# Optimization experiments

Hardware: AMD Instinct MI355X
Metric: run time of the kernel (lower is better)

Reference implementation:

```python
import jax, jax.numpy as jnp
import numpy as np

B, NL, EL, D, H = 16, 512, 1024, 256, 8
HD = D // H
EPS = 1e-5


def _layernorm(x, g, b):
    mu = jnp.mean(x, axis=-1, keepdims=True)
    var = jnp.mean(jnp.square(x - mu), axis=-1, keepdims=True)
    return (x - mu) * jax.lax.rsqrt(var + EPS) * g + b


def setup_inputs() -> dict:
    key = jax.random.key(0)
    ks = jax.random.split(key, 12)
    # xavier-uniform-ish scale for projections
    def xavier(k, shape):
        fan_in, fan_out = shape[0], shape[1]
        lim = float(np.sqrt(6.0 / (fan_in + fan_out)))
        return jax.random.uniform(k, shape, jnp.float32, -lim, lim)
    return {
        "node_x": jax.random.normal(ks[0], (B, NL, D), jnp.float32),
        "edge_x": jax.random.normal(ks[1], (B, EL, D), jnp.float32),
        "node_mask": jnp.zeros((B, NL, NL + EL), dtype=bool),
        "W1": xavier(ks[2], (D, 3 * D)),
        "b1": jnp.zeros((3 * D,), jnp.float32),
        "W2": xavier(ks[3], (D, 2 * D)),
        "b2": jnp.zeros((2 * D,), jnp.float32),
        "lin1_w": xavier(ks[4], (D, D)),
        "lin1_b": jnp.zeros((D,), jnp.float32),
        "lin2_w": xavier(ks[5], (D, D)),
        "lin2_b": jnp.zeros((D,), jnp.float32),
        "ln1_g": jnp.ones((D,), jnp.float32),
        "ln1_b": jnp.zeros((D,), jnp.float32),
        "ln2_g": jnp.ones((D,), jnp.float32),
        "ln2_b": jnp.zeros((D,), jnp.float32),
    }


def reference(node_x, edge_x, node_mask, W1, b1, W2, b2,
              lin1_w, lin1_b, lin2_w, lin2_b, ln1_g, ln1_b, ln2_g, ln2_b):
    b, nl, d = node_x.shape
    el = edge_x.shape[1]
    scaling = float(HD) ** -0.5
    # projections (batch-first; equivalent to the seq-first torch code)
    qkv = node_x @ W1 + b1                       # [b, nl, 3d]
    q, k_node, v_node = jnp.split(qkv, 3, axis=-1)
    kv_e = edge_x @ W2 + b2                      # [b, el, 2d]
    k_edge, v_edge = jnp.split(kv_e, 2, axis=-1)
    k = jnp.concatenate([k_node, k_edge], axis=1)  # [b, nl+el, d]
    v = jnp.concatenate([v_node, v_edge], axis=1)
    # split heads
    qh = q.reshape(b, nl, H, HD)
    kh = k.reshape(b, nl + el, H, HD)
    vh = v.reshape(b, nl + el, H, HD)
    scores = jnp.einsum('bqhd,bkhd->bhqk', qh, kh) * scaling  # [b,h,nl,nl+el]
    scores = jnp.where(node_mask[:, None, :, :], -jnp.inf, scores)
    attn = jax.nn.softmax(scores, axis=-1)
    ctx = jnp.einsum('bhqk,bkhd->bqhd', attn, vh).reshape(b, nl, d)
    # residual + LN1 (dropout is identity in eval/p=0)
    x = _layernorm(node_x + ctx, ln1_g, ln1_b)
    # FFN (relu) + residual + LN2; torch Linear: y = x @ W.T + b
    ff = jax.nn.relu(x @ lin1_w.T + lin1_b) @ lin2_w.T + lin2_b
    x = _layernorm(x + ff, ln2_g, ln2_b)
    return x
```

## Files before the change

### kernel.cpp

```cpp
#include <hip/hip_runtime.h>
#include <hip/hip_bf16.h>

using u16 = unsigned short;
using u32 = unsigned int;
using u64 = unsigned long long;
typedef __attribute__((ext_vector_type(8))) short short8;
typedef __attribute__((ext_vector_type(4))) float f32x4;
typedef __attribute__((ext_vector_type(16))) float f32x16;
typedef __attribute__((ext_vector_type(4))) u32 u32x4;

constexpr int kB = 16, kNL = 512, kEL = 1024, kD = 256, kH = 8, kHD = 32;
constexpr int kS = kNL + kEL;
constexpr int kM1 = kB * kNL;
constexpr float kScale = 0.17677669529663687f;
constexpr float kLog2e = 1.4426950408889634f;
constexpr float kQS = kScale * kLog2e;
constexpr float kEps = 1e-5f;

__device__ __forceinline__ u16 f2bh(float f) {
    __hip_bfloat16 h = __float2bfloat16(f);
    return __builtin_bit_cast(u16, h);
}
__device__ __forceinline__ u32 packbf(float lo, float hi) {
    return (__float_as_uint(hi) & 0xffff0000u) | (__float_as_uint(lo) >> 16);
}
__device__ __forceinline__ void load4(const float* p, float* o) {
    float4 v = *reinterpret_cast<const float4*>(p);
    o[0] = v.x; o[1] = v.y; o[2] = v.z; o[3] = v.w;
}
__device__ __forceinline__ f32x16 fzero16() {
    f32x16 z;
    #pragma unroll
    for (int i = 0; i < 16; ++i) z[i] = 0.f;
    return z;
}

__global__ __launch_bounds__(256) void prep_k(
    const float* __restrict__ W1, const float* __restrict__ W2,
    const float* __restrict__ l1w, const float* __restrict__ l2w,
    const float* __restrict__ nodef, const float* __restrict__ edgef,
    const u32* __restrict__ mask,
    u16* __restrict__ Wt1, u16* __restrict__ Wt2,
    u16* __restrict__ Wt3, u16* __restrict__ Wt4,
    u16* __restrict__ nodeb, u16* __restrict__ edgeb,
    u32* __restrict__ Mw)
{
    const int vb = blockIdx.x, t = threadIdx.x;
    if (vb < 320) {
        const int sec = (vb < 192) ? 0 : 1;
        const int bid = (sec == 0) ? vb : vb - 192;
        const int N = (sec == 0) ? 768 : 512;
        const float* src = (sec == 0) ? W1 : W2;
        u16* dst = (sec == 0) ? Wt1 : Wt2;
        const int tk = bid / (N / 32), tn = bid % (N / 32);
        __shared__ float T[32][33];
        {
            const int k = t >> 3, n4 = (t & 7) * 4;
            float v[4]; load4(src + (size_t)(tk * 32 + k) * N + tn * 32 + n4, v);
            T[n4+0][k] = v[0]; T[n4+1][k] = v[1]; T[n4+2][k] = v[2]; T[n4+3][k] = v[3];
        }
        __syncthreads();
        {
            const int n = t >> 3, k4 = (t & 7) * 4;
            ushort4 o = {f2bh(T[n][k4+0]), f2bh(T[n][k4+1]),
                         f2bh(T[n][k4+2]), f2bh(T[n][k4+3])};
            *reinterpret_cast<ushort4*>(dst + (size_t)(tn*32 + n) * 256 + tk*32 + k4) = o;
        }
        return;
    }
    if (vb < 448) {
        const int sec = (vb < 384) ? 0 : 1;
        const int bid = (sec == 0) ? vb - 320 : vb - 384;
        const float* src = (sec == 0) ? l1w : l2w;
        u16* dst = (sec == 0) ? Wt3 : Wt4;
        const int i = bid * 1024 + t * 4;
        float v[4]; load4(src + i, v);
        ushort4 o = {f2bh(v[0]), f2bh(v[1]), f2bh(v[2]), f2bh(v[3])};
        *reinterpret_cast<ushort4*>(dst + i) = o;
        return;
    }
    if (vb < 6592) {
        const int sec = (vb < 2496) ? 0 : 1;
        const int bid = (sec == 0) ? vb - 448 : vb - 2496;
        const float* src = (sec == 0) ? nodef : edgef;
        u16* dst = (sec == 0) ? nodeb : edgeb;
        const int i = bid * 1024 + t * 4;
        float v[4]; load4(src + i, v);
        ushort4 o = {f2bh(v[0]), f2bh(v[1]), f2bh(v[2]), f2bh(v[3])};
        *reinterpret_cast<ushort4*>(dst + i) = o;
        return;
    }
    {
        const int bid = vb - 6592;
        const int row = bid * 4 + (t >> 6);
        const int l = t & 63;
        const u32* mr = mask + (size_t)row * (kS / 4);
        u32 word = 0;
        #pragma unroll
        for (int k = 0; k < 6; ++k) {
            const u32 v = mr[k * 64 + l];
            const u64 bal = __ballot(v != 0);
            word |= (((bal) & 0xffffull) ? 1u : 0u) << (k * 4 + 0);
            word |= (((bal >> 16) & 0xffffull) ? 1u : 0u) << (k * 4 + 1);
            word |= (((bal >> 32) & 0xffffull) ? 1u : 0u) << (k * 4 + 2);
            word |= (((bal >> 48) & 0xffffull) ? 1u : 0u) << (k * 4 + 3);
        }
        if (l == 0) Mw[row] = word;
    }
}

template<int N, int K, int MODE>
__device__ __forceinline__ void gemm_body128(
    const u16* __restrict__ A, const u16* __restrict__ Wt,
    const float* __restrict__ bias,
    void* __restrict__ o0v, void* __restrict__ o1v, void* __restrict__ o2v,
    int bx, int by, u16* AsB, u16* BsB)
{
    const int t = threadIdx.x;
    const int w = t >> 6, l = t & 63;
    const int wr = w >> 1, wc = w & 1;
    const int lq = l & 15, lg = l >> 4;
    const int bm = bx * 128, bn = by * 128;

    f32x4 acc[4][4];
    #pragma unroll
    for (int mi = 0; mi < 4; ++mi)
        #pragma unroll
        for (int ni = 0; ni < 4; ++ni) acc[mi][ni] = (f32x4){0.f, 0.f, 0.f, 0.f};

    auto stage = [&](int buf, int kk) {
        u16* As = AsB + buf * (128 * 40);
        u16* Bs = BsB + buf * (128 * 40);
        const int m = t >> 1, kh = (t & 1) * 16;
        const u16* ap = A + (size_t)(bm + m) * K + kk + kh;
        *reinterpret_cast<short8*>(&As[m * 40 + kh]) = *reinterpret_cast<const short8*>(ap);
        *reinterpret_cast<short8*>(&As[m * 40 + kh + 8]) = *reinterpret_cast<const short8*>(ap + 8);
        const u16* bp = Wt + (size_t)(bn + m) * K + kk + kh;
        *reinterpret_cast<short8*>(&Bs[m * 40 + kh]) = *reinterpret_cast<const short8*>(bp);
        *reinterpret_cast<short8*>(&Bs[m * 40 + kh + 8]) = *reinterpret_cast<const short8*>(bp + 8);
    };

    stage(0, 0);
    __syncthreads();
    int buf = 0;
    for (int kk = 0; kk < K; kk += 32) {
        if (kk + 32 < K) stage(buf ^ 1, kk + 32);
        const u16* As = AsB + buf * (128 * 40);
        const u16* Bs = BsB + buf * (128 * 40);
        short8 bf[4];
        #pragma unroll
        for (int ni = 0; ni < 4; ++ni)
            bf[ni] = *reinterpret_cast<const short8*>(
                &Bs[(wc * 64 + ni * 16 + lq) * 40 + lg * 8]);
        #pragma unroll
        for (int mi = 0; mi < 4; ++mi) {
            const short8 af = *reinterpret_cast<const short8*>(
                &As[(wr * 64 + mi * 16 + lq) * 40 + lg * 8]);
            #pragma unroll
            for (int ni = 0; ni < 4; ++ni)
                acc[mi][ni] = __builtin_amdgcn_mfma_f32_16x16x32_bf16(
                    af, bf[ni], acc[mi][ni], 0, 0, 0);
        }
        __syncthreads();
        buf ^= 1;
    }

    #pragma unroll
    for (int mi = 0; mi < 4; ++mi) {
        #pragma unroll
        for (int ni = 0; ni < 4; ++ni) {
            const int cg = bn + wc * 64 + ni * 16 + lq;
            const int rg0 = bm + wr * 64 + mi * 16 + lg * 4;
            const float bv = bias[cg];
            float y[4];
            #pragma unroll
            for (int r = 0; r < 4; ++r) y[r] = acc[mi][ni][r] + bv;
            if constexpr (MODE == 0) {
                u16* qo = (u16*)o0v; u16* ko = (u16*)o1v; u16* vt = (u16*)o2v;
                const int bidx = rg0 >> 9, key = rg0 & 511;
                if (cg < 256) {
                    #pragma unroll
                    for (int r = 0; r < 4; ++r)
                        qo[(size_t)(rg0 + r) * kD + cg] = f2bh(y[r] * kQS);
                } else if (cg < 512) {
                    #pragma unroll
                    for (int r = 0; r < 4; ++r)
                        ko[((size_t)bidx * kS + key + r) * kD + (cg - 256)] = f2bh(y[r]);
                } else {
                    const int d0 = cg - 512, hh = d0 >> 5, dd = d0 & 31;
                    ushort4 o = {f2bh(y[0]), f2bh(y[1]), f2bh(y[2]), f2bh(y[3])};
                    *reinterpret_cast<ushort4*>(
                        vt + ((size_t)(bidx * kH + hh) * kHD + dd) * kS + key) = o;
                }
            } else {
                u16* ko = (u16*)o0v; u16* vt = (u16*)o1v;
                const int bidx = rg0 >> 10, key = kNL + (rg0 & 1023);
                if (cg < 256) {
                    #pragma unroll
                    for (int r = 0; r < 4; ++r)
                        ko[((size_t)bidx * kS + key + r) * kD + cg] = f2bh(y[r]);
                } else {
                    const int d0 = cg - 256, hh = d0 >> 5, dd = d0 & 31;
                    ushort4 o = {f2bh(y[0]), f2bh(y[1]), f2bh(y[2]), f2bh(y[3])};
                    *reinterpret_cast<ushort4*>(
                        vt + ((size_t)(bidx * kH + hh) * kHD + dd) * kS + key) = o;
                }
            }
        }
    }
}

__global__ __launch_bounds__(256) void qkv_both(
    const u16* __restrict__ nxb, const u16* __restrict__ exb,
    const u16* __restrict__ wt1, const u16* __restrict__ wt2,
    const float* __restrict__ b1, const float* __restrict__ b2,
    u16* __restrict__ qb, u16* __restrict__ kb, u16* __restrict__ vt)
{
    __shared__ u16 AsB[2 * 128 * 40];
    __shared__ u16 BsB[2 * 128 * 40];
    const int bid = blockIdx.x;
    if (bid < 384) {
        gemm_body128<768, 256, 0>(nxb, wt1, b1, qb, kb, vt,
                                  bid & 63, bid >> 6, AsB, BsB);
    } else {
        const int r = bid - 384;
        gemm_body128<512, 256, 1>(exb, wt2, b2, kb, vt, nullptr,
                                  r & 127, r >> 7, AsB, BsB);
    }
}

__global__ __launch_bounds__(256) void ffn1_k(
    const u16* __restrict__ A, const u16* __restrict__ Wt,
    const float* __restrict__ bias, u16* __restrict__ out)
{
    __shared__ u16 AsB[2][64 * 40];
    __shared__ u16 BsB[2][128 * 40];
    const int t = threadIdx.x;
    const int w = t >> 6, l = t & 63;
    const int wr = w >> 1, wc = w & 1;
    const int lq = l & 15, lg = l >> 4;
    const int bm = blockIdx.x * 64, bn = blockIdx.y * 128;
    constexpr int K = 256;

    f32x4 acc[2][4];
    #pragma unroll
    for (int mi = 0; mi < 2; ++mi)
        #pragma unroll
        for (int ni = 0; ni < 4; ++ni) acc[mi][ni] = (f32x4){0.f, 0.f, 0.f, 0.f};

    auto stage = [&](int buf, int kk) {
        {
            const int m = t >> 2, kq = (t & 3) * 8;
            *reinterpret_cast<short8*>(&AsB[buf][m * 40 + kq]) =
                *reinterpret_cast<const short8*>(A + (size_t)(bm + m) * K + kk + kq);
        }
        {
            const int n = t >> 1, kh = (t & 1) * 16;
            const u16* bp = Wt + (size_t)(bn + n) * K + kk + kh;
            *reinterpret_cast<short8*>(&BsB[buf][n * 40 + kh]) =
                *reinterpret_cast<const short8*>(bp);
            *reinterpret_cast<short8*>(&BsB[buf][n * 40 + kh + 8]) =
                *reinterpret_cast<const short8*>(bp + 8);
        }
    };

    stage(0, 0);
    __syncthreads();
    int buf = 0;
    for (int kk = 0; kk < K; kk += 32) {
        if (kk + 32 < K) stage(buf ^ 1, kk + 32);
        short8 bf[4];
        #pragma unroll
        for (int ni = 0; ni < 4; ++ni)
            bf[ni] = *reinterpret_cast<const short8*>(
                &BsB[buf][(wc * 64 + ni * 16 + lq) * 40 + lg * 8]);
        #pragma unroll
        for (int mi = 0; mi < 2; ++mi) {
            const short8 af = *reinterpret_cast<const short8*>(
                &AsB[buf][(wr * 32 + mi * 16 + lq) * 40 + lg * 8]);
            #pragma unroll
            for (int ni = 0; ni < 4; ++ni)
                acc[mi][ni] = __builtin_amdgcn_mfma_f32_16x16x32_bf16(
                    af, bf[ni], acc[mi][ni], 0, 0, 0);
        }
        __syncthreads();
        buf ^= 1;
    }

    #pragma unroll
    for (int mi = 0; mi < 2; ++mi) {
        #pragma unroll
        for (int ni = 0; ni < 4; ++ni) {
            const int cg = bn + wc * 64 + ni * 16 + lq;
            const int rg0 = bm + wr * 32 + mi * 16 + lg * 4;
            const float bv = bias[cg];
            #pragma unroll
            for (int r = 0; r < 4; ++r)
                out[(size_t)(rg0 + r) * 256 + cg] = f2bh(fmaxf(acc[mi][ni][r] + bv, 0.f));
        }
    }
}

__global__ __launch_bounds__(256) void ffn2_ln2_k(
    const u16* __restrict__ A, const u16* __restrict__ Wt,
    const float* __restrict__ bias, const float* __restrict__ xb,
    const float* __restrict__ gam, const float* __restrict__ bet,
    float* __restrict__ out)
{
    __shared__ __align__(16) char smem[46080];
    u16* AsB = (u16*)smem;
    u16* BsB = (u16*)(smem + 2 * 32 * 40 * 2);
    float* lnb = (float*)smem;
    const int t = threadIdx.x;
    const int w = t >> 6, l = t & 63;
    const int wr = w >> 1, wc = w & 1;
    const int lq = l & 15, lg = l >> 4;
    const int bm = blockIdx.x * 32;
    constexpr int K = 256;

    f32x4 acc[8];
    #pragma unroll
    for (int ni = 0; ni < 8; ++ni) acc[ni] = (f32x4){0.f, 0.f, 0.f, 0.f};

    auto stage = [&](int buf, int kk) {
        {
            const int m = t >> 3, kq = (t & 7) * 4;
            *reinterpret_cast<ushort4*>(&AsB[buf * 32 * 40 + m * 40 + kq]) =
                *reinterpret_cast<const ushort4*>(A + (size_t)(bm + m) * K + kk + kq);
        }
        {
            const int n = t;
            const u16* bp = Wt + (size_t)n * K + kk;
            u16* dst = &BsB[buf * 256 * 40 + n * 40];
            #pragma unroll
            for (int j = 0; j < 4; ++j)
                *reinterpret_cast<short8*>(dst + j * 8) =
                    *reinterpret_cast<const short8*>(bp + j * 8);
        }
    };

    stage(0, 0);
    __syncthreads();
    int buf = 0;
    for (int kk = 0; kk < K; kk += 32) {
        if (kk + 32 < K) stage(buf ^ 1, kk + 32);
        short8 bf[8];
        #pragma unroll
        for (int ni = 0; ni < 8; ++ni)
            bf[ni] = *reinterpret_cast<const short8*>(
                &BsB[buf * 256 * 40 + (wc * 128 + ni * 16 + lq) * 40 + lg * 8]);
        const short8 af = *reinterpret_cast<const short8*>(
            &AsB[buf * 32 * 40 + (wr * 16 + lq) * 40 + lg * 8]);
        #pragma unroll
        for (int ni = 0; ni < 8; ++ni)
            acc[ni] = __builtin_amdgcn_mfma_f32_16x16x32_bf16(af, bf[ni], acc[ni], 0, 0, 0);
        __syncthreads();
        buf ^= 1;
    }

    #pragma unroll
    for (int ni = 0; ni < 8; ++ni) {
        const int cg = wc * 128 + ni * 16 + lq;
        const int rl0 = wr * 16 + lg * 4;
        const float bv = bias[cg];
        #pragma unroll
        for (int r = 0; r < 4; ++r)
            lnb[(rl0 + r) * 260 + cg] = acc[ni][r] + bv;
    }
    __syncthreads();

    #pragma unroll
    for (int rr = 0; rr < 8; ++rr) {
        const int rl = w * 8 + rr;
        const int row = bm + rl;
        float xv[4];
        float4 yv = *reinterpret_cast<const float4*>(&lnb[rl * 260 + l * 4]);
        float rv[4];
        load4(xb + (size_t)row * kD + l * 4, rv);
        xv[0] = yv.x + rv[0]; xv[1] = yv.y + rv[1];
        xv[2] = yv.z + rv[2]; xv[3] = yv.w + rv[3];
        float s = xv[0] + xv[1] + xv[2] + xv[3];
        float q = xv[0]*xv[0] + xv[1]*xv[1] + xv[2]*xv[2] + xv[3]*xv[3];
        #pragma unroll
        for (int off = 1; off < 64; off <<= 1) {
            s += __shfl_xor(s, off);
            q += __shfl_xor(q, off);
        }
        const float mean = s * (1.0f / kD);
        const float var = q * (1.0f / kD) - mean * mean;
        const float rs = rsqrtf(var + kEps);
        float gv[4], bv[4];
        load4(gam + l * 4, gv);
        load4(bet + l * 4, bv);
        float4 o;
        o.x = (xv[0] - mean) * rs * gv[0] + bv[0];
        o.y = (xv[1] - mean) * rs * gv[1] + bv[1];
        o.z = (xv[2] - mean) * rs * gv[2] + bv[2];
        o.w = (xv[3] - mean) * rs * gv[3] + bv[3];
        *reinterpret_cast<float4*>(out + (size_t)row * kD + l * 4) = o;
    }
}

__global__ __launch_bounds__(256) void attn_mfma(
    const u16* __restrict__ Qb, const u16* __restrict__ Kb,
    const u16* __restrict__ VTb, const unsigned char* __restrict__ mask,
    const u32* __restrict__ Mw, float* __restrict__ O)
{
    __shared__ float mba[4][64][17];
    __shared__ float mbb[4][64][17];
    const int t = threadIdx.x;
    const int w = t >> 6, l = t & 63;
    const int q32 = l & 31, hi = l >> 5;
    const int bid = blockIdx.x;
    const int h = bid & 7;
    const int qt = (bid >> 3) & 7;
    const int b = bid >> 6;
    const int qra = qt * 64 + q32;
    const int qrb = qra + 32;

    const u16* qpa = Qb + ((size_t)(b * kNL) + qra) * kD + h * kHD;
    const u16* qpb = Qb + ((size_t)(b * kNL) + qrb) * kD + h * kHD;
    const short8 qf0a = *reinterpret_cast<const short8*>(qpa + hi * 8);
    const short8 qf1a = *reinterpret_cast<const short8*>(qpa + 16 + hi * 8);
    const short8 qf0b = *reinterpret_cast<const short8*>(qpb + hi * 8);
    const short8 qf1b = *reinterpret_cast<const short8*>(qpb + 16 + hi * 8);

    const u16* kbase  = Kb  + ((size_t)b * kS) * kD + h * kHD;
    const u16* vtbase = VTb + ((size_t)(b * kH + h) * kHD) * kS;
    const unsigned char* mra = mask + ((size_t)(b * kNL) + qra) * kS;
    const unsigned char* mrb = mask + ((size_t)(b * kNL) + qrb) * kS;
    const u32 mbitsa = Mw[b * kNL + qra];
    const u32 mbitsb = Mw[b * kNL + qrb];

    f32x16 acca = fzero16(), accb = fzero16();
    float la = 0.f, lb = 0.f;

#define HALFG(kfA, kfB, vfA, vfB, keyh, QF0, QF1, ACC, LRUN, COLD, MROW) do {  \
        f32x16 s = __builtin_amdgcn_mfma_f32_32x32x16_bf16(kfA, QF0, fzero16(), 0, 0, 0); \
        s = __builtin_amdgcn_mfma_f32_32x32x16_bf16(kfB, QF1, s, 0, 0, 0);     \
        float e[16];                                                           \
        _Pragma("unroll")                                                      \
        for (int n = 0; n < 16; ++n) e[n] = __builtin_amdgcn_exp2f(s[n]);      \
        if (COLD) {                                                            \
            _Pragma("unroll")                                                  \
            for (int n = 0; n < 16; ++n) {                                     \
                const int key = (keyh) + (n & 3) + 8 * (n >> 2) + 4 * hi;      \
                if (MROW[key]) e[n] = 0.f;                                     \
            }                                                                  \
        }                                                                      \
        u32 pk[8];                                                             \
        _Pragma("unroll")                                                      \
        for (int qd = 0; qd < 4; ++qd) {                                       \
            LRUN += (e[4*qd] + e[4*qd+1]) + (e[4*qd+2] + e[4*qd+3]);           \
            pk[2*qd]   = packbf(e[4*qd],   e[4*qd+1]);                         \
            pk[2*qd+1] = packbf(e[4*qd+2], e[4*qd+3]);                         \
        }                                                                      \
        {                                                                      \
            u32 xa = pk[0], ya = pk[2], xb_ = pk[1], yb_ = pk[3];              \
            asm("v_permlane32_swap_b32 %0, %1" : "+v"(xa), "+v"(ya));          \
            asm("v_permlane32_swap_b32 %0, %1" : "+v"(xb_), "+v"(yb_));        \
            const short8 pb = __builtin_bit_cast(short8, (u32x4){xa, xb_, ya, yb_}); \
            __builtin_amdgcn_s_setprio(1);                                     \
            ACC = __builtin_amdgcn_mfma_f32_32x32x16_bf16(vfA, pb, ACC, 0, 0, 0); \
            __builtin_amdgcn_s_setprio(0);                                     \
        }                                                                      \
        {                                                                      \
            u32 xa = pk[4], ya = pk[6], xb_ = pk[5], yb_ = pk[7];              \
            asm("v_permlane32_swap_b32 %0, %1" : "+v"(xa), "+v"(ya));          \
            asm("v_permlane32_swap_b32 %0, %1" : "+v"(xb_), "+v"(yb_));        \
            const short8 pb = __builtin_bit_cast(short8, (u32x4){xa, xb_, ya, yb_}); \
            __builtin_amdgcn_s_setprio(1);                                     \
            ACC = __builtin_amdgcn_mfma_f32_32x32x16_bf16(vfB, pb, ACC, 0, 0, 0); \
            __builtin_amdgcn_s_setprio(0);                                     \
        }                                                                      \
} while (0)

    const int ktBeg = w * 6, ktEnd = ktBeg + 6;
    for (int kt = ktBeg; kt < ktEnd; ++kt) {
        const int key0 = kt * 64;
        const u16* krow = kbase + (size_t)(key0 + q32) * kD + hi * 8;
        const u16* vrow = vtbase + (size_t)q32 * kS + key0 + hi * 8;
        const short8 a0 = *reinterpret_cast<const short8*>(krow);
        const short8 a1 = *reinterpret_cast<const short8*>(krow + 16);
        const short8 a2 = *reinterpret_cast<const short8*>(krow + 32 * kD);
        const short8 a3 = *reinterpret_cast<const short8*>(krow + 32 * kD + 16);
        const short8 v0 = *reinterpret_cast<const short8*>(vrow);
        const short8 v1 = *reinterpret_cast<const short8*>(vrow + 16);
        const short8 v2 = *reinterpret_cast<const short8*>(vrow + 32);
        const short8 v3 = *reinterpret_cast<const short8*>(vrow + 48);
        const bool colda = __any(((mbitsa >> kt) & 1u) != 0u);
        const bool coldb = __any(((mbitsb >> kt) & 1u) != 0u);
        HALFG(a0, a1, v0, v1, key0, qf0a, qf1a, acca, la, colda, mra);
        HALFG(a0, a1, v0, v1, key0, qf0b, qf1b, accb, lb, coldb, mrb);
        HALFG(a2, a3, v2, v3, key0 + 32, qf0a, qf1a, acca, la, colda, mra);
        HALFG(a2, a3, v2, v3, key0 + 32, qf0b, qf1b, accb, lb, coldb, mrb);
    }
#undef HALFG

    la += __shfl_xor(la, 32);
    lb += __shfl_xor(lb, 32);

    mba[w][l][0] = la;
    mbb[w][l][0] = lb;
    #pragma unroll
    for (int j = 0; j < 16; ++j) { mba[w][l][1 + j] = acca[j]; mbb[w][l][1 + j] = accb[j]; }
    __syncthreads();
    if (w == 0) {
        {
            float lt = la;
            float ov[16];
            #pragma unroll
            for (int i = 0; i < 16; ++i) ov[i] = acca[i];
            #pragma unroll
            for (int j = 1; j < 4; ++j) {
                lt += mba[j][l][0];
                #pragma unroll
                for (int i = 0; i < 16; ++i) ov[i] += mba[j][l][1 + i];
            }
            const float inv = (lt > 0.f) ? 1.f / lt : 0.f;
            float* orow = O + ((size_t)(b * kNL) + qra) * kD + h * kHD;
            #pragma unroll
            for (int qd = 0; qd < 4; ++qd) {
                float4 o = {ov[4*qd+0] * inv, ov[4*qd+1] * inv,
                            ov[4*qd+2] * inv, ov[4*qd+3] * inv};
                *reinterpret_cast<float4*>(orow + qd * 8 + 4 * hi) = o;
            }
        }
        {
            float lt = lb;
            float ov[16];
            #pragma unroll
            for (int i = 0; i < 16; ++i) ov[i] = accb[i];
            #pragma unroll
            for (int j = 1; j < 4; ++j) {
                lt += mbb[j][l][0];
                #pragma unroll
                for (int i = 0; i < 16; ++i) ov[i] += mbb[j][l][1 + i];
            }
            const float inv = (lt > 0.f) ? 1.f / lt : 0.f;
            float* orow = O + ((size_t)(b * kNL) + qrb) * kD + h * kHD;
            #pragma unroll
            for (int qd = 0; qd < 4; ++qd) {
                float4 o = {ov[4*qd+0] * inv, ov[4*qd+1] * inv,
                            ov[4*qd+2] * inv, ov[4*qd+3] * inv};
                *reinterpret_cast<float4*>(orow + qd * 8 + 4 * hi) = o;
            }
        }
    }
}

__global__ __launch_bounds__(256) void ln_k(
    const float* __restrict__ a_, const float* __restrict__ r,
    const float* __restrict__ gam, const float* __restrict__ bet,
    float* __restrict__ out_, u16* __restrict__ outh)
{
    const int row = blockIdx.x * 4 + (threadIdx.x >> 6);
    const int lane = threadIdx.x & 63;
    const size_t base = (size_t)row * kD + lane * 4;
    float xv[4];
    load4(a_ + base, xv);
    float rv[4];
    load4(r + base, rv);
    #pragma unroll
    for (int t = 0; t < 4; ++t) xv[t] += rv[t];
    float s = xv[0] + xv[1] + xv[2] + xv[3];
    float q = xv[0]*xv[0] + xv[1]*xv[1] + xv[2]*xv[2] + xv[3]*xv[3];
    #pragma unroll
    for (int off = 1; off < 64; off <<= 1) {
        s += __shfl_xor(s, off);
        q += __shfl_xor(q, off);
    }
    const float mean = s * (1.0f / kD);
    const float var = q * (1.0f / kD) - mean * mean;
    const float rs = rsqrtf(var + kEps);
    float gv[4], bv[4];
    load4(gam + lane * 4, gv);
    load4(bet + lane * 4, bv);
    float y[4];
    #pragma unroll
    for (int t = 0; t < 4; ++t) y[t] = (xv[t] - mean) * rs * gv[t] + bv[t];
    float4 o = {y[0], y[1], y[2], y[3]};
    *reinterpret_cast<float4*>(out_ + base) = o;
    ushort4 ob = {f2bh(y[0]), f2bh(y[1]), f2bh(y[2]), f2bh(y[3])};
    *reinterpret_cast<ushort4*>(outh + base) = ob;
}

extern "C" void kernel_launch(void* const* d_in, const int* in_sizes, int n_in,
                              void* d_out, int out_size, void* d_ws, size_t ws_size,
                              hipStream_t stream)
{
    const float* node_x = (const float*)d_in[0];
    const float* edge_x = (const float*)d_in[1];
    const unsigned char* mask = (const unsigned char*)d_in[2];
    const float* W1  = (const float*)d_in[3];
    const float* b1  = (const float*)d_in[4];
    const float* W2  = (const float*)d_in[5];
    const float* b2  = (const float*)d_in[6];
    const float* l1w = (const float*)d_in[7];
    const float* l1b = (const float*)d_in[8];
    const float* l2w = (const float*)d_in[9];
    const float* l2b = (const float*)d_in[10];
    const float* g1  = (const float*)d_in[11];
    const float* be1 = (const float*)d_in[12];
    const float* g2  = (const float*)d_in[13];
    const float* be2 = (const float*)d_in[14];

    char* w = (char*)d_ws;
    u16*   qb  = (u16*)(w);
    u16*   wt1 = (u16*)(w + (4u<<20));
    u16*   wt2 = (u16*)(w + (4u<<20) + 393216);
    u16*   wt3 = (u16*)(w + (4u<<20) + 655360);
    u16*   wt4 = (u16*)(w + (4u<<20) + 786432);
    u32*   mw  = (u32*)(w + (4u<<20) + 917504);
    u16*   nxb = (u16*)(w + (5u<<20));
    u16*   exb = (u16*)(w + (9u<<20));
    u16*   kb  = (u16*)(w + (17u<<20));
    u16*   vt  = (u16*)(w + (30u<<20));
    float* cx  = (float*)(w + (43u<<20));
    float* xb  = (float*)(w + (52u<<20));
    u16*   xbh = exb;
    u16*   fh  = qb;

    prep_k<<<8640, 256, 0, stream>>>(
        W1, W2, l1w, l2w, node_x, edge_x, (const u32*)mask,
        wt1, wt2, wt3, wt4, nxb, exb, mw);
    qkv_both<<<896, 256, 0, stream>>>(nxb, exb, wt1, wt2, b1, b2, qb, kb, vt);
    attn_mfma<<<kB * kH * 8, 256, 0, stream>>>(qb, kb, vt, mask, mw, cx);
    ln_k<<<kM1 / 4, 256, 0, stream>>>(node_x, cx, g1, be1, xb, xbh);
    ffn1_k<<<dim3(kM1 / 64, 2), 256, 0, stream>>>(xbh, wt3, l1b, fh);
    ffn2_ln2_k<<<kM1 / 32, 256, 0, stream>>>(fh, wt4, l2b, xb, g2, be2, (float*)d_out);
}
```

Before: 91.28 us.

## Share K/V tiles across waves via double-buffered LDS in attention kernel

Restructures attention so each block of 8 waves covers 256 queries of one head, with every wave sweeping all keys for its own 32 queries. K and V tiles are staged cooperatively into double-buffered shared memory, and the cross-wave split-K reduction is removed. This cuts redundant global K/V loads per query and eliminates the final LDS reduction. In exchange it adds a barrier per key tile, halves per-wave query work, and launches far fewer blocks, which may lower occupancy.

```diff
diff --git a/kernel.cpp b/kernel.cpp
--- a/kernel.cpp
+++ b/kernel.cpp
@@ -401,57 +401,65 @@
     }
 }
 
-__global__ __launch_bounds__(256) void attn_mfma(
+__global__ __launch_bounds__(512) void attn_mfma(
     const u16* __restrict__ Qb, const u16* __restrict__ Kb,
     const u16* __restrict__ VTb, const unsigned char* __restrict__ mask,
     const u32* __restrict__ Mw, float* __restrict__ O)
 {
-    __shared__ float mba[4][64][17];
-    __shared__ float mbb[4][64][17];
+    __shared__ u16 Ks[2][64 * 40];
+    __shared__ u16 Vs[2][32 * 72];
     const int t = threadIdx.x;
     const int w = t >> 6, l = t & 63;
     const int q32 = l & 31, hi = l >> 5;
     const int bid = blockIdx.x;
     const int h = bid & 7;
-    const int qt = (bid >> 3) & 7;
-    const int b = bid >> 6;
-    const int qra = qt * 64 + q32;
-    const int qrb = qra + 32;
-
-    const u16* qpa = Qb + ((size_t)(b * kNL) + qra) * kD + h * kHD;
-    const u16* qpb = Qb + ((size_t)(b * kNL) + qrb) * kD + h * kHD;
-    const short8 qf0a = *reinterpret_cast<const short8*>(qpa + hi * 8);
-    const short8 qf1a = *reinterpret_cast<const short8*>(qpa + 16 + hi * 8);
-    const short8 qf0b = *reinterpret_cast<const short8*>(qpb + hi * 8);
-    const short8 qf1b = *reinterpret_cast<const short8*>(qpb + 16 + hi * 8);
+    const int half = (bid >> 3) & 1;
+    const int b = bid >> 4;
+    const int qrow = half * 256 + w * 32 + q32;
+
+    const u16* qp = Qb + ((size_t)(b * kNL) + qrow) * kD + h * kHD;
+    const short8 qf0 = *reinterpret_cast<const short8*>(qp + hi * 8);
+    const short8 qf1 = *reinterpret_cast<const short8*>(qp + 16 + hi * 8);
 
     const u16* kbase  = Kb  + ((size_t)b * kS) * kD + h * kHD;
     const u16* vtbase = VTb + ((size_t)(b * kH + h) * kHD) * kS;
-    const unsigned char* mra = mask + ((size_t)(b * kNL) + qra) * kS;
-    const unsigned char* mrb = mask + ((size_t)(b * kNL) + qrb) * kS;
-    const u32 mbitsa = Mw[b * kNL + qra];
-    const u32 mbitsb = Mw[b * kNL + qrb];
-
-    f32x16 acca = fzero16(), accb = fzero16();
-    float la = 0.f, lb = 0.f;
-
-#define HALFG(kfA, kfB, vfA, vfB, keyh, QF0, QF1, ACC, LRUN, COLD, MROW) do {  \
-        f32x16 s = __builtin_amdgcn_mfma_f32_32x32x16_bf16(kfA, QF0, fzero16(), 0, 0, 0); \
-        s = __builtin_amdgcn_mfma_f32_32x32x16_bf16(kfB, QF1, s, 0, 0, 0);     \
+    const unsigned char* mrow = mask + ((size_t)(b * kNL) + qrow) * kS;
+    const u32 mbits = Mw[b * kNL + qrow];
+
+    f32x16 acc = fzero16();
+    float l_run = 0.f;
+
+    auto stage = [&](int buf, int kt) {
+        const int key0 = kt * 64;
+        if (t < 256) {
+            const int r = t >> 2, c = t & 3;
+            *reinterpret_cast<short8*>(&Ks[buf][r * 40 + c * 8]) =
+                *reinterpret_cast<const short8*>(kbase + (size_t)(key0 + r) * kD + c * 8);
+        } else {
+            const int idx = t - 256;
+            const int r = idx >> 3, c = idx & 7;
+            *reinterpret_cast<short8*>(&Vs[buf][r * 72 + c * 8]) =
+                *reinterpret_cast<const short8*>(vtbase + (size_t)r * kS + key0 + c * 8);
+        }
+    };
+
+#define HALFG(kfA, kfB, vfA, vfB, keyh) do {                                   \
+        f32x16 s = __builtin_amdgcn_mfma_f32_32x32x16_bf16(kfA, qf0, fzero16(), 0, 0, 0); \
+        s = __builtin_amdgcn_mfma_f32_32x32x16_bf16(kfB, qf1, s, 0, 0, 0);     \
         float e[16];                                                           \
         _Pragma("unroll")                                                      \
         for (int n = 0; n < 16; ++n) e[n] = __builtin_amdgcn_exp2f(s[n]);      \
-        if (COLD) {                                                            \
+        if (cold) {                                                            \
             _Pragma("unroll")                                                  \
             for (int n = 0; n < 16; ++n) {                                     \
                 const int key = (keyh) + (n & 3) + 8 * (n >> 2) + 4 * hi;      \
-                if (MROW[key]) e[n] = 0.f;                                     \
+                if (mrow[key]) e[n] = 0.f;                                     \
             }                                                                  \
         }                                                                      \
         u32 pk[8];                                                             \
         _Pragma("unroll")                                                      \
         for (int qd = 0; qd < 4; ++qd) {                                       \
-            LRUN += (e[4*qd] + e[4*qd+1]) + (e[4*qd+2] + e[4*qd+3]);           \
+            l_run += (e[4*qd] + e[4*qd+1]) + (e[4*qd+2] + e[4*qd+3]);          \
             pk[2*qd]   = packbf(e[4*qd],   e[4*qd+1]);                         \
             pk[2*qd+1] = packbf(e[4*qd+2], e[4*qd+3]);                         \
         }                                                                      \
@@ -461,7 +469,7 @@
             asm("v_permlane32_swap_b32 %0, %1" : "+v"(xb_), "+v"(yb_));        \
             const short8 pb = __builtin_bit_cast(short8, (u32x4){xa, xb_, ya, yb_}); \
             __builtin_amdgcn_s_setprio(1);                                     \
-            ACC = __builtin_amdgcn_mfma_f32_32x32x16_bf16(vfA, pb, ACC, 0, 0, 0); \
+            acc = __builtin_amdgcn_mfma_f32_32x32x16_bf16(vfA, pb, acc, 0, 0, 0); \
             __builtin_amdgcn_s_setprio(0);                                     \
         }                                                                      \
         {                                                                      \
@@ -470,82 +478,41 @@
             asm("v_permlane32_swap_b32 %0, %1" : "+v"(xb_), "+v"(yb_));        \
             const short8 pb = __builtin_bit_cast(short8, (u32x4){xa, xb_, ya, yb_}); \
             __builtin_amdgcn_s_setprio(1);                                     \
-            ACC = __builtin_amdgcn_mfma_f32_32x32x16_bf16(vfB, pb, ACC, 0, 0, 0); \
+            acc = __builtin_amdgcn_mfma_f32_32x32x16_bf16(vfB, pb, acc, 0, 0, 0); \
             __builtin_amdgcn_s_setprio(0);                                     \
         }                                                                      \
 } while (0)
 
-    const int ktBeg = w * 6, ktEnd = ktBeg + 6;
-    for (int kt = ktBeg; kt < ktEnd; ++kt) {
+    stage(0, 0);
+    __syncthreads();
+    int buf = 0;
+    for (int kt = 0; kt < 24; ++kt) {
+        if (kt + 1 < 24) stage(buf ^ 1, kt + 1);
         const int key0 = kt * 64;
-        const u16* krow = kbase + (size_t)(key0 + q32) * kD + hi * 8;
-        const u16* vrow = vtbase + (size_t)q32 * kS + key0 + hi * 8;
-        const short8 a0 = *reinterpret_cast<const short8*>(krow);
-        const short8 a1 = *reinterpret_cast<const short8*>(krow + 16);
-        const short8 a2 = *reinterpret_cast<const short8*>(krow + 32 * kD);
-        const short8 a3 = *reinterpret_cast<const short8*>(krow + 32 * kD + 16);
-        const short8 v0 = *reinterpret_cast<const short8*>(vrow);
-        const short8 v1 = *reinterpret_cast<const short8*>(vrow + 16);
-        const short8 v2 = *reinterpret_cast<const short8*>(vrow + 32);
-        const short8 v3 = *reinterpret_cast<const short8*>(vrow + 48);
-        const bool colda = __any(((mbitsa >> kt) & 1u) != 0u);
-        const bool coldb = __any(((mbitsb >> kt) & 1u) != 0u);
-        HALFG(a0, a1, v0, v1, key0, qf0a, qf1a, acca, la, colda, mra);
-        HALFG(a0, a1, v0, v1, key0, qf0b, qf1b, accb, lb, coldb, mrb);
-        HALFG(a2, a3, v2, v3, key0 + 32, qf0a, qf1a, acca, la, colda, mra);
-        HALFG(a2, a3, v2, v3, key0 + 32, qf0b, qf1b, accb, lb, coldb, mrb);
+        const bool cold = __any(((mbits >> kt) & 1u) != 0u);
+        const short8 a0 = *reinterpret_cast<const short8*>(&Ks[buf][q32 * 40 + hi * 8]);
+        const short8 a1 = *reinterpret_cast<const short8*>(&Ks[buf][q32 * 40 + 16 + hi * 8]);
+        const short8 a2 = *reinterpret_cast<const short8*>(&Ks[buf][(32 + q32) * 40 + hi * 8]);
+        const short8 a3 = *reinterpret_cast<const short8*>(&Ks[buf][(32 + q32) * 40 + 16 + hi * 8]);
+        const short8 v0 = *reinterpret_cast<const short8*>(&Vs[buf][q32 * 72 + hi * 8]);
+        const short8 v1 = *reinterpret_cast<const short8*>(&Vs[buf][q32 * 72 + 16 + hi * 8]);
+        const short8 v2 = *reinterpret_cast<const short8*>(&Vs[buf][q32 * 72 + 32 + hi * 8]);
+        const short8 v3 = *reinterpret_cast<const short8*>(&Vs[buf][q32 * 72 + 48 + hi * 8]);
+        HALFG(a0, a1, v0, v1, key0);
+        HALFG(a2, a3, v2, v3, key0 + 32);
+        __syncthreads();
+        buf ^= 1;
     }
 #undef HALFG
 
-    la += __shfl_xor(la, 32);
-    lb += __shfl_xor(lb, 32);
-
-    mba[w][l][0] = la;
-    mbb[w][l][0] = lb;
-    #pragma unroll
-    for (int j = 0; j < 16; ++j) { mba[w][l][1 + j] = acca[j]; mbb[w][l][1 + j] = accb[j]; }
-    __syncthreads();
-    if (w == 0) {
-        {
-            float lt = la;
-            float ov[16];
-            #pragma unroll
-            for (int i = 0; i < 16; ++i) ov[i] = acca[i];
-            #pragma unroll
-            for (int j = 1; j < 4; ++j) {
-                lt += mba[j][l][0];
-                #pragma unroll
-                for (int i = 0; i < 16; ++i) ov[i] += mba[j][l][1 + i];
-            }
-            const float inv = (lt > 0.f) ? 1.f / lt : 0.f;
-            float* orow = O + ((size_t)(b * kNL) + qra) * kD + h * kHD;
-            #pragma unroll
-            for (int qd = 0; qd < 4; ++qd) {
-                float4 o = {ov[4*qd+0] * inv, ov[4*qd+1] * inv,
-                            ov[4*qd+2] * inv, ov[4*qd+3] * inv};
-                *reinterpret_cast<float4*>(orow + qd * 8 + 4 * hi) = o;
-            }
-        }
-        {
-            float lt = lb;
-            float ov[16];
-            #pragma unroll
-            for (int i = 0; i < 16; ++i) ov[i] = accb[i];
-            #pragma unroll
-            for (int j = 1; j < 4; ++j) {
-                lt += mbb[j][l][0];
-                #pragma unroll
-                for (int i = 0; i < 16; ++i) ov[i] += mbb[j][l][1 + i];
-            }
-            const float inv = (lt > 0.f) ? 1.f / lt : 0.f;
-            float* orow = O + ((size_t)(b * kNL) + qrb) * kD + h * kHD;
-            #pragma unroll
-            for (int qd = 0; qd < 4; ++qd) {
-                float4 o = {ov[4*qd+0] * inv, ov[4*qd+1] * inv,
-                            ov[4*qd+2] * inv, ov[4*qd+3] * inv};
-                *reinterpret_cast<float4*>(orow + qd * 8 + 4 * hi) = o;
-            }
-        }
+    l_run += __shfl_xor(l_run, 32);
+    const float inv = (l_run > 0.f) ? 1.f / l_run : 0.f;
+    float* orow = O + ((size_t)(b * kNL) + qrow) * kD + h * kHD;
+    #pragma unroll
+    for (int qd = 0; qd < 4; ++qd) {
+        float4 o = {acc[4*qd+0] * inv, acc[4*qd+1] * inv,
+                    acc[4*qd+2] * inv, acc[4*qd+3] * inv};
+        *reinterpret_cast<float4*>(orow + qd * 8 + 4 * hi) = o;
     }
 }
 
@@ -625,7 +592,7 @@
         W1, W2, l1w, l2w, node_x, edge_x, (const u32*)mask,
         wt1, wt2, wt3, wt4, nxb, exb, mw);
     qkv_both<<<896, 256, 0, stream>>>(nxb, exb, wt1, wt2, b1, b2, qb, kb, vt);
-    attn_mfma<<<kB * kH * 8, 256, 0, stream>>>(qb, kb, vt, mask, mw, cx);
+    attn_mfma<<<kB * 2 * 8, 512, 0, stream>>>(qb, kb, vt, mask, mw, cx);
     ln_k<<<kM1 / 4, 256, 0, stream>>>(node_x, cx, g1, be1, xb, xbh);
     ffn1_k<<<dim3(kM1 / 64, 2), 256, 0, stream>>>(xbh, wt3, l1b, fh);
     ffn2_ln2_k<<<kM1 / 32, 256, 0, stream>>>(fh, wt4, l2b, xb, g2, be2, (float*)d_out);
```

Result: no change. 91.98 us (+0.8%).
